# Kernel tuning notes

Hardware: AMD Instinct MI355X
Metric: run time of the kernel (lower is better)

The kernel has to match this reference:

```python
import jax, jax.numpy as jnp
import numpy as np

L = 2        # n_layers
IN = 172     # in_channels
HID = 128    # hidden_channels
NH = 4       # heads
HD = HID // NH  # per-head dim = 32
TD = 100     # time_dim
V = 400000   # global node table size
N = 150000   # sampled subgraph nodes
E = 500000   # edges per layer
B = 15000    # seed batch size


def setup_inputs() -> dict:
    key = jax.random.key(0)
    ks = jax.random.split(key, 24)
    p = lambda k, shp, s=0.05: jax.random.normal(k, shp, jnp.float32) * s
    inp = {
        "x_all": jax.random.normal(ks[0], (V, IN), jnp.float32),
        "all_node_ids": jax.random.randint(ks[1], (N,), 0, V),
        "edge_src": jax.random.randint(ks[2], (L, E), 0, N),
        "edge_dst": jax.random.randint(ks[3], (L, E), 0, N),
        "dts": jax.random.uniform(ks[4], (L, E), jnp.float32, 0.0, 1e4),
        "batch_size": B,
        # TimeEncode params
        "basis_freq": jnp.asarray(1.0 / 10 ** np.linspace(0, 9, TD), jnp.float32),
        "phase": jnp.zeros((TD,), jnp.float32),
        # input projection
        "Wp": p(ks[5], (IN, HID)), "bp": jnp.zeros((HID,), jnp.float32),
        # per-layer TransformerConv params (stacked over L)
        "Wq": p(ks[6], (L, HID, HID)), "bq": jnp.zeros((L, HID), jnp.float32),
        "Wk": p(ks[7], (L, HID, HID)), "bk": jnp.zeros((L, HID), jnp.float32),
        "Wv": p(ks[8], (L, HID, HID)), "bv": jnp.zeros((L, HID), jnp.float32),
        "We": p(ks[9], (L, TD, HID)),  # lin_edge, bias=False in PyG
        "Wskip": p(ks[10], (L, HID, HID)), "bskip": jnp.zeros((L, HID), jnp.float32),
        "bn_g": jnp.ones((L, HID), jnp.float32), "bn_b": jnp.zeros((L, HID), jnp.float32),
        # classifier head
        "W1": p(ks[11], (HID, HID)), "b1": jnp.zeros((HID,), jnp.float32),
        "g1": jnp.ones((HID,), jnp.float32), "be1": jnp.zeros((HID,), jnp.float32),
        "W2": p(ks[12], (HID, HID // 2)), "b2": jnp.zeros((HID // 2,), jnp.float32),
        "g2": jnp.ones((HID // 2,), jnp.float32), "be2": jnp.zeros((HID // 2,), jnp.float32),
        "W3": p(ks[13], (HID // 2, 1)), "b3": jnp.zeros((1,), jnp.float32),
    }
    return inp


def _bn(x, g, b):
    # BatchNorm1d, training-mode batch statistics (biased variance), eps=1e-5
    m = x.mean(0)
    v = x.var(0)
    return g * (x - m) * jax.lax.rsqrt(v + 1e-5) + b


def reference(x_all, all_node_ids, edge_src, edge_dst, dts, batch_size,
              basis_freq, phase, Wp, bp, Wq, bq, Wk, bk, Wv, bv, We,
              Wskip, bskip, bn_g, bn_b, W1, b1, g1, be1, W2, b2, g2, be2, W3, b3):
    n = all_node_ids.shape[0]
    x = x_all[all_node_ids]                      # [N, IN] gather from global table
    h = jax.nn.relu(x @ Wp + bp)                 # [N, HID]
    inv_sqrt_d = 1.0 / np.sqrt(HD)
    for i in range(L):
        src, dst, dt = edge_src[i], edge_dst[i], dts[i]
        # learnable sinusoidal time encoding of edge delta-t  [E, TD]
        te = jnp.cos(dt[:, None] * basis_freq[None, :] + phase[None, :])
        q = (h @ Wq[i] + bq[i]).reshape(n, NH, HD)
        k = (h @ Wk[i] + bk[i]).reshape(n, NH, HD)
        v = (h @ Wv[i] + bv[i]).reshape(n, NH, HD)
        e = (te @ We[i]).reshape(-1, NH, HD)     # [E, NH, HD]
        kj = k[src] + e                          # key + edge proj (PyG TransformerConv)
        vj = v[src] + e                          # value + edge proj
        alpha = jnp.einsum('ehd,ehd->eh', q[dst], kj) * inv_sqrt_d  # [E, NH]
        # scatter-softmax over edges grouped by destination node
        m = jax.ops.segment_max(alpha, dst, num_segments=n)
        a = jnp.exp(alpha - m[dst])
        s = jax.ops.segment_sum(a, dst, num_segments=n) + 1e-16
        w = a / s[dst]                           # [E, NH]
        agg = jax.ops.segment_sum(w[:, :, None] * vj, dst, num_segments=n)
        out = agg.reshape(n, HID) + h @ Wskip[i] + bskip[i]  # concat heads + root skip
        h = _bn(jax.nn.relu(out), bn_g[i], bn_b[i])          # dropout = identity (eval)
    hb = h[:batch_size]
    z = jax.nn.relu(_bn(hb @ W1 + b1, g1, be1))
    z = jax.nn.relu(_bn(z @ W2 + b2, g2, be2))
    return (z @ W3 + b3)[:, 0]                   # [batch_size]
```

## Files before the change

kernel.cpp:

```cpp
#include <hip/hip_runtime.h>
#include <hip/hip_bf16.h>
#include <math.h>

#define IN_DIM 172
#define HID 128
#define TDIM 100
#define KPAD 192

typedef __attribute__((ext_vector_type(8))) short bf16x8;
typedef __attribute__((ext_vector_type(4))) float f32x4;

static __device__ __forceinline__ ushort f2b(float x) {
  unsigned u = __float_as_uint(x);
  u += 0x7FFFu + ((u >> 16) & 1u);
  return (ushort)(u >> 16);
}
static __device__ __forceinline__ float blo(unsigned w) { return __uint_as_float(w << 16); }
static __device__ __forceinline__ float bhi(unsigned w) { return __uint_as_float(w & 0xffff0000u); }
static __device__ __forceinline__ float b2f(ushort v) { return __uint_as_float((unsigned)v << 16); }

__global__ void k_prep(const float* __restrict__ Wp,
                       const float* __restrict__ Wq, const float* __restrict__ Wk,
                       const float* __restrict__ Wv, const float* __restrict__ Ws,
                       const float* __restrict__ bq, const float* __restrict__ bk,
                       const float* __restrict__ bv, const float* __restrict__ bs,
                       const float* __restrict__ We, const float* __restrict__ W1,
                       ushort* __restrict__ wpt,
                       ushort* __restrict__ wallT0, ushort* __restrict__ wallT1,
                       float* __restrict__ ball0, float* __restrict__ ball1,
                       ushort* __restrict__ wet0, ushort* __restrict__ wet1,
                       ushort* __restrict__ w1t) {
  int i = blockIdx.x * 256 + threadIdx.x;
  if (i < 128 * KPAD) {
    int c = i / KPAD, k = i - c * KPAD;
    wpt[i] = (k < IN_DIM) ? f2b(Wp[k * HID + c]) : (ushort)0;
    return;
  }
  i -= 128 * KPAD;
  if (i < 2 * 512 * 128) {
    int layer = i >> 16;
    int j = i & 65535;
    int col = j >> 7, k = j & 127;
    int m = col >> 7, c = col & 127;
    const float* W = (m == 0) ? Wq : (m == 1) ? Wk : (m == 2) ? Wv : Ws;
    W += (size_t)layer * HID * HID;
    (layer ? wallT1 : wallT0)[j] = f2b(W[k * HID + c]);
    if (k == 0) {
      const float* bb = (m == 0) ? bq : (m == 1) ? bk : (m == 2) ? bv : bs;
      (layer ? ball1 : ball0)[col] = bb[layer * HID + c];
    }
    return;
  }
  i -= 2 * 512 * 128;
  if (i < 2 * 128 * 128) {
    int layer = i >> 14;
    int j = i & 16383;
    int c = j >> 7, t = j & 127;
    (layer ? wet1 : wet0)[j] =
        (t < TDIM) ? f2b(We[((size_t)layer * TDIM + t) * HID + c]) : (ushort)0;
    return;
  }
  i -= 2 * 128 * 128;
  if (i < 128 * 128) {
    int c = i >> 7, k = i & 127;
    w1t[i] = f2b(W1[k * HID + c]);
  }
}

__global__ __launch_bounds__(256) void k_in_mfma(
    const float* __restrict__ x_all, const int* __restrict__ ids,
    const ushort* __restrict__ wpt, const float* __restrict__ bp,
    ushort* __restrict__ h, int n) {
  __shared__ __align__(16) ushort xs[64][200];
  int tid = threadIdx.x;
  long r0 = (long)blockIdx.x * 64;
  for (int i = tid; i < 64 * 28; i += 256) {
    int r = i / 28, c = IN_DIM + (i - r * 28);
    xs[r][c] = 0;
  }
  for (int i = tid; i < 64 * 43; i += 256) {
    int r = i / 43, seg = i - r * 43;
    long row = r0 + r;
    float4 v = make_float4(0.f, 0.f, 0.f, 0.f);
    if (row < n) v = *(const float4*)(x_all + (size_t)ids[row] * IN_DIM + seg * 4);
    ushort4 u;
    u.x = f2b(v.x); u.y = f2b(v.y); u.z = f2b(v.z); u.w = f2b(v.w);
    *(ushort4*)&xs[r][seg * 4] = u;
  }
  __syncthreads();
  int wv = tid >> 6, l = tid & 63;
  int arow = wv * 16 + (l & 15);
  int kb0 = (l >> 4) * 8;
  bf16x8 a[6];
  #pragma unroll
  for (int kk = 0; kk < 6; ++kk) a[kk] = *(const bf16x8*)&xs[arow][kk * 32 + kb0];
  #pragma unroll
  for (int nt = 0; nt < 8; ++nt) {
    int col = nt * 16 + (l & 15);
    const ushort* wcol = wpt + (size_t)col * KPAD + kb0;
    f32x4 acc = {0.f, 0.f, 0.f, 0.f};
    #pragma unroll
    for (int kk = 0; kk < 6; ++kk) {
      bf16x8 bfr = *(const bf16x8*)(wcol + kk * 32);
      acc = __builtin_amdgcn_mfma_f32_16x16x32_bf16(a[kk], bfr, acc, 0, 0, 0);
    }
    float bias = bp[col];
    #pragma unroll
    for (int j = 0; j < 4; ++j) {
      long row = r0 + wv * 16 + (l >> 4) * 4 + j;
      if (row < n) {
        float y = acc[j] + bias;
        h[row * HID + col] = f2b(y > 0.f ? y : 0.f);
      }
    }
  }
}

template <bool BN_IN>
__global__ __launch_bounds__(512) void k_qkvs(
    const ushort* __restrict__ hbf, const ushort* __restrict__ xf,
    const float* __restrict__ sums, const float* __restrict__ bng,
    const float* __restrict__ bnb, float inv_n,
    const ushort* __restrict__ wallT, const float* __restrict__ ball,
    ushort* __restrict__ qb, ushort* __restrict__ kvb,
    ushort* __restrict__ ob, int n) {
  __shared__ __align__(16) ushort hs[128][136];
  __shared__ float As[128], Bs[128];
  int tid = threadIdx.x;
  if (BN_IN) {
    if (tid < 128) {
      float mean = sums[tid] * inv_n;
      float var = sums[128 + tid] * inv_n - mean * mean;
      float A = bng[tid] * rsqrtf(var + 1e-5f);
      As[tid] = A;
      Bs[tid] = bnb[tid] - mean * A;
    }
    __syncthreads();
  }
  long r0 = (long)blockIdx.x * 128;
  for (int i = tid; i < 128 * 16; i += 512) {
    int r = i >> 4, cseg = i & 15;
    long row = r0 + r;
    int c0 = cseg * 8;
    if (BN_IN) {
      ushort4 ua = {0, 0, 0, 0}, ub = {0, 0, 0, 0};
      if (row < n) {
        uint4 xw = *(const uint4*)(xf + row * HID + c0);
        float x0 = blo(xw.x), x1 = bhi(xw.x), x2 = blo(xw.y), x3 = bhi(xw.y);
        float x4 = blo(xw.z), x5 = bhi(xw.z), x6 = blo(xw.w), x7 = bhi(xw.w);
        ua.x = f2b(As[c0 + 0] * fmaxf(x0, 0.f) + Bs[c0 + 0]);
        ua.y = f2b(As[c0 + 1] * fmaxf(x1, 0.f) + Bs[c0 + 1]);
        ua.z = f2b(As[c0 + 2] * fmaxf(x2, 0.f) + Bs[c0 + 2]);
        ua.w = f2b(As[c0 + 3] * fmaxf(x3, 0.f) + Bs[c0 + 3]);
        ub.x = f2b(As[c0 + 4] * fmaxf(x4, 0.f) + Bs[c0 + 4]);
        ub.y = f2b(As[c0 + 5] * fmaxf(x5, 0.f) + Bs[c0 + 5]);
        ub.z = f2b(As[c0 + 6] * fmaxf(x6, 0.f) + Bs[c0 + 6]);
        ub.w = f2b(As[c0 + 7] * fmaxf(x7, 0.f) + Bs[c0 + 7]);
      }
      *(ushort4*)&hs[r][c0] = ua;
      *(ushort4*)&hs[r][c0 + 4] = ub;
    } else {
      bf16x8 zv = {0, 0, 0, 0, 0, 0, 0, 0};
      bf16x8 v = (row < n) ? *(const bf16x8*)&hbf[row * HID + c0] : zv;
      *(bf16x8*)&hs[r][c0] = v;
    }
  }
  int wv = tid >> 6, l = tid & 63;
  int kb0 = (l >> 4) * 8;
  int Cw = wv * 64;
  int m = wv >> 1;
  bf16x8 b[4][4];
  float bias4[4];
  #pragma unroll
  for (int ct = 0; ct < 4; ++ct) {
    int col = Cw + ct * 16 + (l & 15);
    bias4[ct] = ball[col];
    #pragma unroll
    for (int kk = 0; kk < 4; ++kk)
      b[ct][kk] = *(const bf16x8*)&wallT[(size_t)col * 128 + kk * 32 + kb0];
  }
  __syncthreads();
  #pragma unroll 2
  for (int rt = 0; rt < 8; ++rt) {
    bf16x8 a[4];
    #pragma unroll
    for (int kk = 0; kk < 4; ++kk)
      a[kk] = *(const bf16x8*)&hs[rt * 16 + (l & 15)][kk * 32 + kb0];
    f32x4 acc[4];
    #pragma unroll
    for (int ct = 0; ct < 4; ++ct) acc[ct] = (f32x4){0.f, 0.f, 0.f, 0.f};
    #pragma unroll
    for (int kk = 0; kk < 4; ++kk) {
      #pragma unroll
      for (int ct = 0; ct < 4; ++ct)
        acc[ct] = __builtin_amdgcn_mfma_f32_16x16x32_bf16(a[kk], b[ct][kk], acc[ct], 0, 0, 0);
    }
    #pragma unroll
    for (int ct = 0; ct < 4; ++ct) {
      int cc = (wv & 1) * 64 + ct * 16 + (l & 15);
      #pragma unroll
      for (int j = 0; j < 4; ++j) {
        long row = r0 + rt * 16 + (l >> 4) * 4 + j;
        if (row < n) {
          float y = acc[ct][j] + bias4[ct];
          if (m == 0) qb[row * HID + cc] = f2b(y);
          else if (m == 1) kvb[row * 256 + cc] = f2b(y);
          else if (m == 2) kvb[row * 256 + 128 + cc] = f2b(y);
          else ob[row * HID + cc] = f2b(y);
        }
      }
    }
  }
}

__global__ __launch_bounds__(256) void k_mfma128_bn(
    const ushort* __restrict__ xf, const float* __restrict__ sums,
    const float* __restrict__ bng, const float* __restrict__ bnb, float inv_n,
    const ushort* __restrict__ WT, const float* __restrict__ bias,
    float* __restrict__ Y, int n) {
  __shared__ __align__(16) ushort hs[64][136];
  __shared__ float As[128], Bs[128];
  int tid = threadIdx.x;
  if (tid < 128) {
    float mean = sums[tid] * inv_n;
    float var = sums[128 + tid] * inv_n - mean * mean;
    float A = bng[tid] * rsqrtf(var + 1e-5f);
    As[tid] = A;
    Bs[tid] = bnb[tid] - mean * A;
  }
  __syncthreads();
  long r0 = (long)blockIdx.x * 64;
  for (int i = tid; i < 64 * 16; i += 256) {
    int r = i >> 4, cseg = i & 15;
    long row = r0 + r;
    int c0 = cseg * 8;
    ushort4 ua = {0, 0, 0, 0}, ub = {0, 0, 0, 0};
    if (row < n) {
      uint4 xw = *(const uint4*)(xf + row * HID + c0);
      float x0 = blo(xw.x), x1 = bhi(xw.x), x2 = blo(xw.y), x3 = bhi(xw.y);
      float x4 = blo(xw.z), x5 = bhi(xw.z), x6 = blo(xw.w), x7 = bhi(xw.w);
      ua.x = f2b(As[c0 + 0] * fmaxf(x0, 0.f) + Bs[c0 + 0]);
      ua.y = f2b(As[c0 + 1] * fmaxf(x1, 0.f) + Bs[c0 + 1]);
      ua.z = f2b(As[c0 + 2] * fmaxf(x2, 0.f) + Bs[c0 + 2]);
      ua.w = f2b(As[c0 + 3] * fmaxf(x3, 0.f) + Bs[c0 + 3]);
      ub.x = f2b(As[c0 + 4] * fmaxf(x4, 0.f) + Bs[c0 + 4]);
      ub.y = f2b(As[c0 + 5] * fmaxf(x5, 0.f) + Bs[c0 + 5]);
      ub.z = f2b(As[c0 + 6] * fmaxf(x6, 0.f) + Bs[c0 + 6]);
      ub.w = f2b(As[c0 + 7] * fmaxf(x7, 0.f) + Bs[c0 + 7]);
    }
    *(ushort4*)&hs[r][c0] = ua;
    *(ushort4*)&hs[r][c0 + 4] = ub;
  }
  __syncthreads();
  int wv = tid >> 6, l = tid & 63;
  int arow = wv * 16 + (l & 15);
  int kb0 = (l >> 4) * 8;
  bf16x8 a[4];
  #pragma unroll
  for (int kk = 0; kk < 4; ++kk) a[kk] = *(const bf16x8*)&hs[arow][kk * 32 + kb0];
  #pragma unroll
  for (int nt = 0; nt < 8; ++nt) {
    int col = nt * 16 + (l & 15);
    const ushort* wcol = WT + (size_t)col * 128 + kb0;
    f32x4 acc = {0.f, 0.f, 0.f, 0.f};
    #pragma unroll
    for (int kk = 0; kk < 4; ++kk) {
      bf16x8 bfr = *(const bf16x8*)(wcol + kk * 32);
      acc = __builtin_amdgcn_mfma_f32_16x16x32_bf16(a[kk], bfr, acc, 0, 0, 0);
    }
    float bs = bias[col];
    #pragma unroll
    for (int j = 0; j < 4; ++j) {
      long row = r0 + wv * 16 + (l >> 4) * 4 + j;
      if (row < n) Y[row * HID + col] = acc[j] + bs;
    }
  }
}

__global__ void k_hist2(const int* __restrict__ dst_all, int* __restrict__ counts,
                        int n, int nE2, int nE) {
  int e = blockIdx.x * 256 + threadIdx.x;
  if (e >= nE2) return;
  int layer = (e >= nE) ? 1 : 0;
  atomicAdd(&counts[layer * n + dst_all[e]], 1);
}

__global__ void k_scan_chunk(const int* __restrict__ counts, int* __restrict__ offs,
                             int* __restrict__ chunkSums, int m) {
  __shared__ int ls[256];
  int t = threadIdx.x;
  int base = blockIdx.x * 1024 + t * 4;
  int v[4];
  #pragma unroll
  for (int j = 0; j < 4; ++j) v[j] = (base + j < m) ? counts[base + j] : 0;
  ls[t] = v[0] + v[1] + v[2] + v[3];
  __syncthreads();
  for (int off = 1; off < 256; off <<= 1) {
    int x = (t >= off) ? ls[t - off] : 0;
    __syncthreads();
    ls[t] += x;
    __syncthreads();
  }
  int run = (t == 0) ? 0 : ls[t - 1];
  if (t == 255) chunkSums[blockIdx.x] = ls[255];
  #pragma unroll
  for (int j = 0; j < 4; ++j) {
    if (base + j < m) offs[base + j] = run;
    run += v[j];
  }
}

__global__ __launch_bounds__(512) void k_scan_tops(int* __restrict__ chunkSums, int nchunks) {
  __shared__ int ls[512];
  int t = threadIdx.x;
  ls[t] = (t < nchunks) ? chunkSums[t] : 0;
  __syncthreads();
  for (int off = 1; off < 512; off <<= 1) {
    int x = (t >= off) ? ls[t - off] : 0;
    __syncthreads();
    ls[t] += x;
    __syncthreads();
  }
  int excl = (t == 0) ? 0 : ls[t - 1];
  if (t < nchunks) chunkSums[t] = excl;
}

__global__ void k_scan_add(int* __restrict__ offs, const int* __restrict__ chunkSums,
                           int m, int totalE) {
  int i = blockIdx.x * 256 + threadIdx.x;
  if (i < m) offs[i] += chunkSums[i >> 10];
  if (i == 0) offs[m] = totalE;
}

__global__ void k_scatter2(const int* __restrict__ src_all, const int* __restrict__ dst_all,
                           const float* __restrict__ dts_all, const int* __restrict__ offs,
                           int* __restrict__ cursor, uint2* __restrict__ edata,
                           int n, int nE2, int nE) {
  int e = blockIdx.x * 256 + threadIdx.x;
  if (e >= nE2) return;
  int layer = (e >= nE) ? 1 : 0;
  int d = layer * n + dst_all[e];
  int pos = offs[d] + atomicAdd(&cursor[d], 1);
  edata[pos] = make_uint2((unsigned)src_all[e], __float_as_uint(dts_all[e]));
}

__global__ __launch_bounds__(256) void k_te_mfma(
    const uint2* __restrict__ edata, const float* __restrict__ freq,
    const float* __restrict__ phase, const ushort* __restrict__ wet,
    ushort* __restrict__ eb, int nE) {
  __shared__ __align__(16) ushort te[64][136];
  __shared__ float dt_s[64];
  __shared__ float fr_s[128], ph_s[128];
  int tid = threadIdx.x;
  if (tid < 128) {
    fr_s[tid] = (tid < TDIM) ? freq[tid] : 0.f;
    ph_s[tid] = (tid < TDIM) ? phase[tid] : 0.f;
  }
  long e0 = (long)blockIdx.x << 6;
  if (tid < 64) dt_s[tid] = (e0 + tid < nE) ? __uint_as_float(edata[e0 + tid].y) : 0.f;
  __syncthreads();
  for (int i = tid; i < 64 * 128; i += 256) {
    int el = i >> 7, t = i & 127;
    float val = (t < TDIM) ? __cosf(dt_s[el] * fr_s[t] + ph_s[t]) : 0.f;
    te[el][t] = f2b(val);
  }
  __syncthreads();
  int wv = tid >> 6, l = tid & 63;
  int arow = wv * 16 + (l & 15);
  int kb0 = (l >> 4) * 8;
  bf16x8 a[4];
  #pragma unroll
  for (int kk = 0; kk < 4; ++kk) a[kk] = *(const bf16x8*)&te[arow][kk * 32 + kb0];
  __syncthreads();
  #pragma unroll
  for (int nt = 0; nt < 8; ++nt) {
    int col = nt * 16 + (l & 15);
    const ushort* wcol = wet + (size_t)col * 128 + kb0;
    f32x4 acc = {0.f, 0.f, 0.f, 0.f};
    #pragma unroll
    for (int kk = 0; kk < 4; ++kk) {
      bf16x8 bfr = *(const bf16x8*)(wcol + kk * 32);
      acc = __builtin_amdgcn_mfma_f32_16x16x32_bf16(a[kk], bfr, acc, 0, 0, 0);
    }
    #pragma unroll
    for (int j = 0; j < 4; ++j)
      te[wv * 16 + (l >> 4) * 4 + j][col] = f2b(acc[j]);
  }
  __syncthreads();
  for (int i = tid; i < 64 * 16; i += 256) {
    int r = i >> 4, cs = i & 15;
    long row = e0 + r;
    if (row < nE) *(bf16x8*)&eb[row * 128 + cs * 8] = *(const bf16x8*)&te[r][cs * 8];
  }
}

__global__ void k_attn(const int* __restrict__ offs_l, const uint2* __restrict__ edata,
                       int bias, const ushort* __restrict__ eb,
                       const ushort* __restrict__ qb, const ushort* __restrict__ kvb,
                       ushort* __restrict__ ob, int n) {
  int d = (blockIdx.x * 256 + threadIdx.x) >> 6;
  if (d >= n) return;
  int lane = threadIdx.x & 63;
  int sub = lane >> 4;
  int cl = lane & 15;
  int c0 = cl * 8;
  int beg = offs_l[d], end = offs_l[d + 1];
  if (beg == end) return;
  const ushort* ebl = eb - (size_t)bias * HID;
  uint4 qw = *(const uint4*)(qb + (size_t)d * HID + c0);
  float q0 = blo(qw.x), q1 = bhi(qw.x), q2 = blo(qw.y), q3 = bhi(qw.y);
  float q4 = blo(qw.z), q5 = bhi(qw.z), q6 = blo(qw.w), q7 = bhi(qw.w);
  float s = 0.f;
  float a0 = 0.f, a1 = 0.f, a2 = 0.f, a3 = 0.f, a4 = 0.f, a5 = 0.f, a6 = 0.f, a7 = 0.f;
  for (int base = beg; base < end; base += 4) {
    int pos = base + sub;
    bool valid = pos < end;
    int pp = valid ? pos : beg;
    int sv = (int)edata[pp].x;
    uint4 kw = *(const uint4*)(kvb + (size_t)sv * 256 + c0);
    uint4 vw = *(const uint4*)(kvb + (size_t)sv * 256 + 128 + c0);
    uint4 ew = *(const uint4*)(ebl + (size_t)pp * HID + c0);
    float e0 = blo(ew.x), e1 = bhi(ew.x), e2 = blo(ew.y), e3 = bhi(ew.y);
    float e4 = blo(ew.z), e5 = bhi(ew.z), e6 = blo(ew.w), e7 = bhi(ew.w);
    float p = q0 * (blo(kw.x) + e0) + q1 * (bhi(kw.x) + e1) +
              q2 * (blo(kw.y) + e2) + q3 * (bhi(kw.y) + e3) +
              q4 * (blo(kw.z) + e4) + q5 * (bhi(kw.z) + e5) +
              q6 * (blo(kw.w) + e6) + q7 * (bhi(kw.w) + e7);
    p += __shfl_xor(p, 1);
    p += __shfl_xor(p, 2);
    float pe = valid ? __expf(p * 0.17677669529663687f) : 0.f;
    s += pe;
    a0 += pe * (blo(vw.x) + e0);
    a1 += pe * (bhi(vw.x) + e1);
    a2 += pe * (blo(vw.y) + e2);
    a3 += pe * (bhi(vw.y) + e3);
    a4 += pe * (blo(vw.z) + e4);
    a5 += pe * (bhi(vw.z) + e5);
    a6 += pe * (blo(vw.w) + e6);
    a7 += pe * (bhi(vw.w) + e7);
  }
  #pragma unroll
  for (int off = 16; off <= 32; off <<= 1) {
    s += __shfl_xor(s, off);
    a0 += __shfl_xor(a0, off); a1 += __shfl_xor(a1, off);
    a2 += __shfl_xor(a2, off); a3 += __shfl_xor(a3, off);
    a4 += __shfl_xor(a4, off); a5 += __shfl_xor(a5, off);
    a6 += __shfl_xor(a6, off); a7 += __shfl_xor(a7, off);
  }
  if (sub == 0) {
    float inv = 1.f / (s + 1e-16f);
    uint4* o = (uint4*)(ob + (size_t)d * HID + c0);
    uint4 ow = *o;
    float y0 = blo(ow.x) + a0 * inv, y1 = bhi(ow.x) + a1 * inv;
    float y2 = blo(ow.y) + a2 * inv, y3 = bhi(ow.y) + a3 * inv;
    float y4 = blo(ow.z) + a4 * inv, y5 = bhi(ow.z) + a5 * inv;
    float y6 = blo(ow.w) + a6 * inv, y7 = bhi(ow.w) + a7 * inv;
    uint4 w;
    w.x = (unsigned)f2b(y0) | ((unsigned)f2b(y1) << 16);
    w.y = (unsigned)f2b(y2) | ((unsigned)f2b(y3) << 16);
    w.z = (unsigned)f2b(y4) | ((unsigned)f2b(y5) << 16);
    w.w = (unsigned)f2b(y6) | ((unsigned)f2b(y7) << 16);
    *o = w;
  }
}

__global__ void k_bn_reduce_b(const ushort* __restrict__ X, int n,
                              float* __restrict__ sums) {
  int col = threadIdx.x & 127;
  int rloc = threadIdx.x >> 7;
  float s = 0.f, s2 = 0.f;
  for (long r = (long)blockIdx.x * 2 + rloc; r < n; r += (long)gridDim.x * 2) {
    float v = b2f(X[r * HID + col]);
    v = v > 0.f ? v : 0.f;
    s += v; s2 += v * v;
  }
  __shared__ float ls[256], ls2[256];
  ls[threadIdx.x] = s; ls2[threadIdx.x] = s2;
  __syncthreads();
  if (rloc == 0) {
    s += ls[128 + col]; s2 += ls2[128 + col];
    atomicAdd(&sums[col], s);
    atomicAdd(&sums[128 + col], s2);
  }
}

__global__ void k_bn_reduce(const float* __restrict__ X, int n, int C, int shift,
                            float* __restrict__ sums) {
  int col = threadIdx.x & (C - 1);
  int rloc = threadIdx.x >> shift;
  int rpt = 256 >> shift;
  float s = 0.f, s2 = 0.f;
  for (long r = (long)blockIdx.x * rpt + rloc; r < n; r += (long)gridDim.x * rpt) {
    float v = X[r * C + col];
    s += v; s2 += v * v;
  }
  __shared__ float ls[256], ls2[256];
  ls[threadIdx.x] = s; ls2[threadIdx.x] = s2;
  __syncthreads();
  if (rloc == 0) {
    for (int j = 1; j < rpt; ++j) { s += ls[j * C + col]; s2 += ls2[j * C + col]; }
    atomicAdd(&sums[col], s);
    atomicAdd(&sums[C + col], s2);
  }
}

__global__ __launch_bounds__(256) void k_gemm_64(
    const float* __restrict__ X, const float* __restrict__ sums,
    const float* __restrict__ g, const float* __restrict__ be, float inv_n,
    const float* __restrict__ W, const float* __restrict__ b,
    float* __restrict__ Y, int n) {
  __shared__ float xs[16][HID];
  __shared__ float As[128], Bs[128];
  if (threadIdx.x < 128) {
    int c = threadIdx.x;
    float mean = sums[c] * inv_n;
    float var = sums[128 + c] * inv_n - mean * mean;
    float A = g[c] * rsqrtf(var + 1e-5f);
    As[c] = A;
    Bs[c] = be[c] - mean * A;
  }
  __syncthreads();
  int r0 = blockIdx.x * 16;
  for (int idx = threadIdx.x; idx < 16 * HID; idx += 256) {
    int r = idx >> 7, c = idx & 127;
    int row = r0 + r;
    float v = (row < n) ? X[(size_t)row * HID + c] : 0.f;
    v = As[c] * v + Bs[c];
    xs[r][c] = v > 0.f ? v : 0.f;
  }
  __syncthreads();
  int col = threadIdx.x & 63;
  int rg = threadIdx.x >> 6;
  float acc[4] = {0.f, 0.f, 0.f, 0.f};
  #pragma unroll 4
  for (int kk = 0; kk < HID; ++kk) {
    float w = W[kk * 64 + col];
    #pragma unroll
    for (int j = 0; j < 4; ++j) acc[j] += xs[rg + 4 * j][kk] * w;
  }
  float bias = b[col];
  #pragma unroll
  for (int j = 0; j < 4; ++j) {
    int row = r0 + rg + 4 * j;
    if (row < n) Y[(size_t)row * 64 + col] = acc[j] + bias;
  }
}

__global__ __launch_bounds__(256) void k_final(
    const float* __restrict__ z2, const float* __restrict__ sums,
    const float* __restrict__ g2, const float* __restrict__ be2, float inv_n,
    const float* __restrict__ W3, const float* __restrict__ b3,
    float* __restrict__ out, int n) {
  int wave = threadIdx.x >> 6, lane = threadIdx.x & 63;
  int row = blockIdx.x * 4 + wave;
  if (row >= n) return;
  float z = z2[(size_t)row * 64 + lane];
  float mean = sums[lane] * inv_n;
  float var = sums[64 + lane] * inv_n - mean * mean;
  float v = g2[lane] * (z - mean) * rsqrtf(var + 1e-5f) + be2[lane];
  v = v > 0.f ? v : 0.f;
  float pv = v * W3[lane];
  pv += __shfl_xor(pv, 1);
  pv += __shfl_xor(pv, 2);
  pv += __shfl_xor(pv, 4);
  pv += __shfl_xor(pv, 8);
  pv += __shfl_xor(pv, 16);
  pv += __shfl_xor(pv, 32);
  if (lane == 0) out[row] = pv + b3[0];
}

extern "C" void kernel_launch(void* const* d_in, const int* in_sizes, int n_in,
                              void* d_out, int out_size, void* d_ws, size_t ws_size,
                              hipStream_t stream) {
  const float* x_all = (const float*)d_in[0];
  const int* ids = (const int*)d_in[1];
  const int* esrc = (const int*)d_in[2];
  const int* edst = (const int*)d_in[3];
  const float* dts = (const float*)d_in[4];
  const float* freq = (const float*)d_in[6];
  const float* phase = (const float*)d_in[7];
  const float* Wp = (const float*)d_in[8];
  const float* bp = (const float*)d_in[9];
  const float* Wq = (const float*)d_in[10];
  const float* bq = (const float*)d_in[11];
  const float* Wk = (const float*)d_in[12];
  const float* bk = (const float*)d_in[13];
  const float* Wv = (const float*)d_in[14];
  const float* bv = (const float*)d_in[15];
  const float* We = (const float*)d_in[16];
  const float* Wskip = (const float*)d_in[17];
  const float* bskip = (const float*)d_in[18];
  const float* bn_g = (const float*)d_in[19];
  const float* bn_b = (const float*)d_in[20];
  const float* W1 = (const float*)d_in[21];
  const float* b1 = (const float*)d_in[22];
  const float* g1 = (const float*)d_in[23];
  const float* be1 = (const float*)d_in[24];
  const float* W2 = (const float*)d_in[25];
  const float* b2 = (const float*)d_in[26];
  const float* g2 = (const float*)d_in[27];
  const float* be2 = (const float*)d_in[28];
  const float* W3 = (const float*)d_in[29];
  const float* b3 = (const float*)d_in[30];

  size_t n = (size_t)in_sizes[1];
  size_t nE = (size_t)in_sizes[2] / 2;
  size_t nE2 = nE * 2;
  int B = out_size;

  char* pc = (char*)d_ws;
  auto alloc = [&](size_t bytes) { char* r = pc; pc += (bytes + 255) & ~(size_t)255; return r; };
  ushort* h    = (ushort*)alloc(n * HID * 2);
  ushort* qb   = (ushort*)alloc(n * HID * 2);
  ushort* kvb  = (ushort*)alloc(n * 256 * 2);
  ushort* ob0  = (ushort*)alloc(n * HID * 2);
  ushort* ob1  = (ushort*)alloc(n * HID * 2);
  ushort* eb0  = (ushort*)alloc(nE * HID * 2);
  ushort* eb1  = (ushort*)alloc(nE * HID * 2);
  uint2* edata = (uint2*)alloc(nE2 * 8);
  int* offs    = (int*)alloc((2 * n + 2) * 4);
  int* chunkS  = (int*)alloc(512 * 4);
  size_t zbytes = 4 * n * 4 + 4 * 256 * 4;
  char* zb = alloc(zbytes);
  int* counts = (int*)zb;
  int* cursor = counts + 2 * n;
  float* sumsL0 = (float*)(cursor + 2 * n);
  float* sumsL1 = sumsL0 + 256;
  float* sumsZ1 = sumsL1 + 256;
  float* sumsZ2 = sumsZ1 + 256;
  ushort* wpt    = (ushort*)alloc(128 * KPAD * 2);
  ushort* wallT0 = (ushort*)alloc(512 * 128 * 2);
  ushort* wallT1 = (ushort*)alloc(512 * 128 * 2);
  float* ball0   = (float*)alloc(512 * 4);
  float* ball1   = (float*)alloc(512 * 4);
  ushort* wet0   = (ushort*)alloc(128 * 128 * 2);
  ushort* wet1   = (ushort*)alloc(128 * 128 * 2);
  ushort* w1t    = (ushort*)alloc(128 * 128 * 2);
  float* z1      = (float*)alloc((size_t)B * HID * 4);
  float* z2      = (float*)alloc((size_t)B * 64 * 4);

  int gn64 = (int)((n + 63) / 64);
  int gn128 = (int)((n + 127) / 128);
  int ge2 = (int)((nE2 + 255) / 256);
  int eblk = (int)((nE + 63) / 64);
  int m2 = (int)(2 * n);
  int nchunks = (m2 + 1023) / 1024;
  float inv_nf = 1.f / (float)n;
  float inv_bf = 1.f / (float)B;

  hipMemsetAsync(zb, 0, zbytes, stream);
  k_prep<<<(128 * KPAD + 2 * 512 * 128 + 2 * 128 * 128 + 128 * 128 + 255) / 256, 256, 0, stream>>>(
      Wp, Wq, Wk, Wv, Wskip, bq, bk, bv, bskip, We, W1,
      wpt, wallT0, wallT1, ball0, ball1, wet0, wet1, w1t);

  k_hist2<<<ge2, 256, 0, stream>>>(edst, counts, (int)n, (int)nE2, (int)nE);
  k_scan_chunk<<<nchunks, 256, 0, stream>>>(counts, offs, chunkS, m2);
  k_scan_tops<<<1, 512, 0, stream>>>(chunkS, nchunks);
  k_scan_add<<<(m2 + 255) / 256, 256, 0, stream>>>(offs, chunkS, m2, (int)nE2);
  k_scatter2<<<ge2, 256, 0, stream>>>(esrc, edst, dts, offs, cursor, edata,
                                      (int)n, (int)nE2, (int)nE);

  k_te_mfma<<<eblk, 256, 0, stream>>>(edata, freq, phase, wet0, eb0, (int)nE);

  k_in_mfma<<<gn64, 256, 0, stream>>>(x_all, ids, wpt, bp, h, (int)n);

  for (int i = 0; i < 2; ++i) {
    const ushort* wallT = i ? wallT1 : wallT0;
    const float* ball = i ? ball1 : ball0;
    const ushort* eb = i ? eb1 : eb0;
    ushort* ob = i ? ob1 : ob0;
    int bias = i * (int)nE;

    if (i == 1)
      k_te_mfma<<<eblk, 256, 0, stream>>>(edata + nE, freq, phase, wet1, eb1, (int)nE);

    if (i == 0)
      k_qkvs<false><<<gn128, 512, 0, stream>>>(h, nullptr, nullptr, nullptr, nullptr, 0.f,
                                               wallT, ball, qb, kvb, ob, (int)n);
    else
      k_qkvs<true><<<gn128, 512, 0, stream>>>(nullptr, ob0, sumsL0, bn_g, bn_b, inv_nf,
                                              wallT, ball, qb, kvb, ob, (int)n);

    k_attn<<<(int)((n + 3) / 4), 256, 0, stream>>>(offs + (size_t)i * n, edata, bias,
                                                   eb, qb, kvb, ob, (int)n);
    k_bn_reduce_b<<<512, 256, 0, stream>>>(ob, (int)n, i ? sumsL1 : sumsL0);
  }

  k_mfma128_bn<<<(B + 63) / 64, 256, 0, stream>>>(ob1, sumsL1, bn_g + HID, bn_b + HID,
                                                  inv_nf, w1t, b1, z1, B);
  k_bn_reduce<<<512, 256, 0, stream>>>(z1, B, HID, 7, sumsZ1);
  k_gemm_64<<<(B + 15) / 16, 256, 0, stream>>>(z1, sumsZ1, g1, be1, inv_bf, W2, b2, z2, B);
  k_bn_reduce<<<512, 256, 0, stream>>>(z2, B, 64, 6, sumsZ2);
  k_final<<<(B + 3) / 4, 256, 0, stream>>>(z2, sumsZ2, g2, be2, inv_bf, W3, b3,
                                           (float*)d_out, B);
}
```

Measured before the change: 1.005 ms.

## Map attention to 16 lanes per node; fuse head BN stats into GEMMs

The attention kernel now gives each destination node 16 lanes that walk its edges one at a time, instead of 64 lanes that split edges four ways. This removes the cross-subgroup shuffle reduction and the lanes wasted on low-degree nodes. The trade-off is divergence, since the four nodes sharing a wave can have different degrees. Separately, the classifier-head GEMM kernels now accumulate per-column sum and sum-of-squares in their epilogues through shared and global atomics, which removes two standalone BN reduction launches.

New measurement: 967.2 us, median of 2. 1.04x faster.

```diff
diff --git a/kernel.cpp b/kernel.cpp
--- a/kernel.cpp
+++ b/kernel.cpp
@@ -217,9 +217,10 @@
     const ushort* __restrict__ xf, const float* __restrict__ sums,
     const float* __restrict__ bng, const float* __restrict__ bnb, float inv_n,
     const ushort* __restrict__ WT, const float* __restrict__ bias,
-    float* __restrict__ Y, int n) {
+    float* __restrict__ Y, float* __restrict__ zsums, int n) {
   __shared__ __align__(16) ushort hs[64][136];
   __shared__ float As[128], Bs[128];
+  __shared__ float zs1[128], zs2[128];
   int tid = threadIdx.x;
   if (tid < 128) {
     float mean = sums[tid] * inv_n;
@@ -227,6 +228,8 @@
     float A = bng[tid] * rsqrtf(var + 1e-5f);
     As[tid] = A;
     Bs[tid] = bnb[tid] - mean * A;
+    zs1[tid] = 0.f;
+    zs2[tid] = 0.f;
   }
   __syncthreads();
   long r0 = (long)blockIdx.x * 64;
@@ -269,11 +272,24 @@
       acc = __builtin_amdgcn_mfma_f32_16x16x32_bf16(a[kk], bfr, acc, 0, 0, 0);
     }
     float bs = bias[col];
+    float ts = 0.f, tss = 0.f;
     #pragma unroll
     for (int j = 0; j < 4; ++j) {
       long row = r0 + wv * 16 + (l >> 4) * 4 + j;
-      if (row < n) Y[row * HID + col] = acc[j] + bs;
-    }
+      if (row < n) {
+        float y = acc[j] + bs;
+        Y[row * HID + col] = y;
+        ts += y;
+        tss += y * y;
+      }
+    }
+    atomicAdd(&zs1[col], ts);
+    atomicAdd(&zs2[col], tss);
+  }
+  __syncthreads();
+  if (tid < 128) {
+    atomicAdd(&zsums[tid], zs1[tid]);
+    atomicAdd(&zsums[128 + tid], zs2[tid]);
   }
 }
 
@@ -398,11 +414,9 @@
                        int bias, const ushort* __restrict__ eb,
                        const ushort* __restrict__ qb, const ushort* __restrict__ kvb,
                        ushort* __restrict__ ob, int n) {
-  int d = (blockIdx.x * 256 + threadIdx.x) >> 6;
+  int d = (blockIdx.x * 256 + threadIdx.x) >> 4;
   if (d >= n) return;
-  int lane = threadIdx.x & 63;
-  int sub = lane >> 4;
-  int cl = lane & 15;
+  int cl = threadIdx.x & 15;
   int c0 = cl * 8;
   int beg = offs_l[d], end = offs_l[d + 1];
   if (beg == end) return;
@@ -412,14 +426,11 @@
   float q4 = blo(qw.z), q5 = bhi(qw.z), q6 = blo(qw.w), q7 = bhi(qw.w);
   float s = 0.f;
   float a0 = 0.f, a1 = 0.f, a2 = 0.f, a3 = 0.f, a4 = 0.f, a5 = 0.f, a6 = 0.f, a7 = 0.f;
-  for (int base = beg; base < end; base += 4) {
-    int pos = base + sub;
-    bool valid = pos < end;
-    int pp = valid ? pos : beg;
-    int sv = (int)edata[pp].x;
+  for (int pos = beg; pos < end; ++pos) {
+    int sv = (int)edata[pos].x;
     uint4 kw = *(const uint4*)(kvb + (size_t)sv * 256 + c0);
     uint4 vw = *(const uint4*)(kvb + (size_t)sv * 256 + 128 + c0);
-    uint4 ew = *(const uint4*)(ebl + (size_t)pp * HID + c0);
+    uint4 ew = *(const uint4*)(ebl + (size_t)pos * HID + c0);
     float e0 = blo(ew.x), e1 = bhi(ew.x), e2 = blo(ew.y), e3 = bhi(ew.y);
     float e4 = blo(ew.z), e5 = bhi(ew.z), e6 = blo(ew.w), e7 = bhi(ew.w);
     float p = q0 * (blo(kw.x) + e0) + q1 * (bhi(kw.x) + e1) +
@@ -428,7 +439,7 @@
               q6 * (blo(kw.w) + e6) + q7 * (bhi(kw.w) + e7);
     p += __shfl_xor(p, 1);
     p += __shfl_xor(p, 2);
-    float pe = valid ? __expf(p * 0.17677669529663687f) : 0.f;
+    float pe = __expf(p * 0.17677669529663687f);
     s += pe;
     a0 += pe * (blo(vw.x) + e0);
     a1 += pe * (bhi(vw.x) + e1);
@@ -439,29 +450,19 @@
     a6 += pe * (blo(vw.w) + e6);
     a7 += pe * (bhi(vw.w) + e7);
   }
-  #pragma unroll
-  for (int off = 16; off <= 32; off <<= 1) {
-    s += __shfl_xor(s, off);
-    a0 += __shfl_xor(a0, off); a1 += __shfl_xor(a1, off);
-    a2 += __shfl_xor(a2, off); a3 += __shfl_xor(a3, off);
-    a4 += __shfl_xor(a4, off); a5 += __shfl_xor(a5, off);
-    a6 += __shfl_xor(a6, off); a7 += __shfl_xor(a7, off);
-  }
-  if (sub == 0) {
-    float inv = 1.f / (s + 1e-16f);
-    uint4* o = (uint4*)(ob + (size_t)d * HID + c0);
-    uint4 ow = *o;
-    float y0 = blo(ow.x) + a0 * inv, y1 = bhi(ow.x) + a1 * inv;
-    float y2 = blo(ow.y) + a2 * inv, y3 = bhi(ow.y) + a3 * inv;
-    float y4 = blo(ow.z) + a4 * inv, y5 = bhi(ow.z) + a5 * inv;
-    float y6 = blo(ow.w) + a6 * inv, y7 = bhi(ow.w) + a7 * inv;
-    uint4 w;
-    w.x = (unsigned)f2b(y0) | ((unsigned)f2b(y1) << 16);
-    w.y = (unsigned)f2b(y2) | ((unsigned)f2b(y3) << 16);
-    w.z = (unsigned)f2b(y4) | ((unsigned)f2b(y5) << 16);
-    w.w = (unsigned)f2b(y6) | ((unsigned)f2b(y7) << 16);
-    *o = w;
-  }
+  float inv = 1.f / (s + 1e-16f);
+  uint4* o = (uint4*)(ob + (size_t)d * HID + c0);
+  uint4 ow = *o;
+  float y0 = blo(ow.x) + a0 * inv, y1 = bhi(ow.x) + a1 * inv;
+  float y2 = blo(ow.y) + a2 * inv, y3 = bhi(ow.y) + a3 * inv;
+  float y4 = blo(ow.z) + a4 * inv, y5 = bhi(ow.z) + a5 * inv;
+  float y6 = blo(ow.w) + a6 * inv, y7 = bhi(ow.w) + a7 * inv;
+  uint4 w;
+  w.x = (unsigned)f2b(y0) | ((unsigned)f2b(y1) << 16);
+  w.y = (unsigned)f2b(y2) | ((unsigned)f2b(y3) << 16);
+  w.z = (unsigned)f2b(y4) | ((unsigned)f2b(y5) << 16);
+  w.w = (unsigned)f2b(y6) | ((unsigned)f2b(y7) << 16);
+  *o = w;
 }
 
 __global__ void k_bn_reduce_b(const ushort* __restrict__ X, int n,
@@ -484,33 +485,14 @@
   }
 }
 
-__global__ void k_bn_reduce(const float* __restrict__ X, int n, int C, int shift,
-                            float* __restrict__ sums) {
-  int col = threadIdx.x & (C - 1);
-  int rloc = threadIdx.x >> shift;
-  int rpt = 256 >> shift;
-  float s = 0.f, s2 = 0.f;
-  for (long r = (long)blockIdx.x * rpt + rloc; r < n; r += (long)gridDim.x * rpt) {
-    float v = X[r * C + col];
-    s += v; s2 += v * v;
-  }
-  __shared__ float ls[256], ls2[256];
-  ls[threadIdx.x] = s; ls2[threadIdx.x] = s2;
-  __syncthreads();
-  if (rloc == 0) {
-    for (int j = 1; j < rpt; ++j) { s += ls[j * C + col]; s2 += ls2[j * C + col]; }
-    atomicAdd(&sums[col], s);
-    atomicAdd(&sums[C + col], s2);
-  }
-}
-
 __global__ __launch_bounds__(256) void k_gemm_64(
     const float* __restrict__ X, const float* __restrict__ sums,
     const float* __restrict__ g, const float* __restrict__ be, float inv_n,
     const float* __restrict__ W, const float* __restrict__ b,
-    float* __restrict__ Y, int n) {
+    float* __restrict__ Y, float* __restrict__ zsums, int n) {
   __shared__ float xs[16][HID];
   __shared__ float As[128], Bs[128];
+  __shared__ float zs1[64], zs2[64];
   if (threadIdx.x < 128) {
     int c = threadIdx.x;
     float mean = sums[c] * inv_n;
@@ -518,6 +500,7 @@
     float A = g[c] * rsqrtf(var + 1e-5f);
     As[c] = A;
     Bs[c] = be[c] - mean * A;
+    if (c < 64) { zs1[c] = 0.f; zs2[c] = 0.f; }
   }
   __syncthreads();
   int r0 = blockIdx.x * 16;
@@ -539,10 +522,23 @@
     for (int j = 0; j < 4; ++j) acc[j] += xs[rg + 4 * j][kk] * w;
   }
   float bias = b[col];
+  float ts = 0.f, tss = 0.f;
   #pragma unroll
   for (int j = 0; j < 4; ++j) {
     int row = r0 + rg + 4 * j;
-    if (row < n) Y[(size_t)row * 64 + col] = acc[j] + bias;
+    if (row < n) {
+      float y = acc[j] + bias;
+      Y[(size_t)row * 64 + col] = y;
+      ts += y;
+      tss += y * y;
+    }
+  }
+  atomicAdd(&zs1[col], ts);
+  atomicAdd(&zs2[col], tss);
+  __syncthreads();
+  if (threadIdx.x < 64) {
+    atomicAdd(&zsums[threadIdx.x], zs1[threadIdx.x]);
+    atomicAdd(&zsums[64 + threadIdx.x], zs2[threadIdx.x]);
   }
 }
 
@@ -681,16 +677,15 @@
       k_qkvs<true><<<gn128, 512, 0, stream>>>(nullptr, ob0, sumsL0, bn_g, bn_b, inv_nf,
                                               wallT, ball, qb, kvb, ob, (int)n);
 
-    k_attn<<<(int)((n + 3) / 4), 256, 0, stream>>>(offs + (size_t)i * n, edata, bias,
-                                                   eb, qb, kvb, ob, (int)n);
+    k_attn<<<(int)((n + 15) / 16), 256, 0, stream>>>(offs + (size_t)i * n, edata, bias,
+                                                     eb, qb, kvb, ob, (int)n);
     k_bn_reduce_b<<<512, 256, 0, stream>>>(ob, (int)n, i ? sumsL1 : sumsL0);
   }
 
   k_mfma128_bn<<<(B + 63) / 64, 256, 0, stream>>>(ob1, sumsL1, bn_g + HID, bn_b + HID,
-                                                  inv_nf, w1t, b1, z1, B);
-  k_bn_reduce<<<512, 256, 0, stream>>>(z1, B, HID, 7, sumsZ1);
-  k_gemm_64<<<(B + 15) / 16, 256, 0, stream>>>(z1, sumsZ1, g1, be1, inv_bf, W2, b2, z2, B);
-  k_bn_reduce<<<512, 256, 0, stream>>>(z2, B, 64, 6, sumsZ2);
+                                                  inv_nf, w1t, b1, z1, sumsZ1, B);
+  k_gemm_64<<<(B + 15) / 16, 256, 0, stream>>>(z1, sumsZ1, g1, be1, inv_bf, W2, b2,
+                                               z2, sumsZ2, B);
   k_final<<<(B + 3) / 4, 256, 0, stream>>>(z2, sumsZ2, g2, be2, inv_bf, W3, b3,
                                            (float*)d_out, B);
 }
```
